# Kernel optimization log

Measured on AMD Instinct MI355X. Metric: run time of the kernel, lower is better.

Reference implementation:

```python
import jax, jax.numpy as jnp
import numpy as np

N = 256          # HiPPO order
DT = 1.0 / 4096  # discretization step ~ 1/L
L, BATCH = 4096, 64
GBT_ALPHA = 0.5  # bilinear transform (matches discretization=0.5)


def _legt_matrices(n):
    # Closed-form HiPPO-LegT transition matrices (Gu et al.), lambda_n=1.
    q = np.arange(n, dtype=np.float64)
    r = (2.0 * q + 1.0) ** 0.5
    j, i = np.meshgrid(q, q)  # i: row index n, j: col index k
    A = -(r[:, None] * np.where(i < j, (-1.0) ** (i - j), 1.0) * r[None, :])
    B = r[:, None]  # (N, 1)
    return A, B


def _discretize_gbt(A, B, dt, alpha):
    # Generalized bilinear transform, identical to scipy cont2discrete('gbt').
    n = A.shape[0]
    I = np.eye(n)
    M = np.linalg.inv(I - dt * alpha * A)
    dA = M @ (I + dt * (1.0 - alpha) * A)
    dB = (M @ (dt * B)).squeeze(-1)
    return dA.astype(np.float32), dB.astype(np.float32)


def setup_inputs() -> dict:
    key = jax.random.key(0)
    A, B = _legt_matrices(N)
    dA, dB = _discretize_gbt(A, B, DT, GBT_ALPHA)
    inputs = jax.random.normal(key, (L, BATCH), dtype=jnp.float32)
    return {"inputs": inputs, "dA": jnp.asarray(dA), "dB": jnp.asarray(dB)}


def reference(inputs, dA, dB):
    # inputs: (L, B); dA: (N, N); dB: (N,)
    # u_t = inputs_t[..., None] * dB  -> (L, B, N)
    u = inputs[..., None] * dB

    def step(c, u_t):
        # c_t = dA @ c_{t-1} + u_t  (row-vector form: c @ dA^T)
        c = c @ dA.T + u_t
        return c, c

    c0 = jnp.zeros(u.shape[1:], dtype=u.dtype)  # (B, N)
    _, cs = jax.lax.scan(step, c0, u)
    return cs  # (L, B, N)
```

## Files before the change

### kernel.cpp

```cpp
#include <hip/hip_runtime.h>
#include <hip/hip_bf16.h>
#include <stdint.h>


#define N 256
#define LSEQ 4096
#define BATCH 64
#define TCH 64
#define NCH 64

#define MG_STRIDE 36

using bf16x8 = __attribute__((ext_vector_type(8))) __bf16;
using f32x4  = __attribute__((ext_vector_type(4))) float;

__device__ __forceinline__ unsigned short f2bf(float f) {
  uint32_t x = __builtin_bit_cast(uint32_t, f);
  uint32_t r = x + 0x7fffu + ((x >> 16) & 1u);
  return (unsigned short)(r >> 16);
}
__device__ __forceinline__ float bf2f(unsigned short h) {
  uint32_t x = ((uint32_t)h) << 16;
  return __builtin_bit_cast(float, x);
}

__device__ __forceinline__ int swz(int r, int c) { return r * 32 + ((c ^ ((r >> 1) & 3)) << 3); }

#define OFF_Phi 16777216
#define OFF_Plo 25165824
#define OFF_Kf  33554432
#define OFF_Khi 33619968
#define OFF_Klo 33652736
#define OFF_shi 33685504
#define OFF_slo 35782656
#define OFF_G0  37879808
#define OFF_uT  42074112
#define OFF_Sqh 43122688
#define OFF_Sql 43778048


__device__ __forceinline__ void mm64_tile(const float* __restrict__ A, const float* __restrict__ B,
                                          float* __restrict__ Cw, unsigned short* __restrict__ Chi,
                                          unsigned short* __restrict__ Clo, int bx, int tid,
                                          char* smem) {
  float (*At)[68] = (float(*)[68])smem;
  float (*Bs)[68] = (float(*)[68])(smem + 4352);
  int gr0 = (bx >> 2) * 64, gc0 = (bx & 3) * 64;
  int ty = tid >> 4, tx = tid & 15;
  float acc[4][4];
  #pragma unroll
  for (int r = 0; r < 4; ++r)
    #pragma unroll
    for (int c = 0; c < 4; ++c) acc[r][c] = 0.f;
  int ra = tid >> 2, ka4 = (tid & 3) << 2;
  int kb = tid >> 4, cb4 = (tid & 15) << 2;
  const float* pa = &A[(size_t)(gr0 + ra) * 256 + ka4];
  const float* pb = &B[(size_t)kb * 256 + gc0 + cb4];
  float4 va = *(const float4*)pa;
  float4 vb = *(const float4*)pb;
  for (int k0 = 0; k0 < 256; k0 += 16) {
    At[ka4 + 0][ra] = va.x; At[ka4 + 1][ra] = va.y;
    At[ka4 + 2][ra] = va.z; At[ka4 + 3][ra] = va.w;
    *(float4*)&Bs[kb][cb4] = vb;
    __syncthreads();
    if (k0 + 16 < 256) {
      va = *(const float4*)(pa + k0 + 16);
      vb = *(const float4*)(pb + (size_t)(k0 + 16) * 256);
    }
    #pragma unroll
    for (int kk = 0; kk < 16; ++kk) {
      float4 a4 = *(const float4*)&At[kk][ty << 2];
      float4 b4 = *(const float4*)&Bs[kk][tx << 2];
      acc[0][0] += a4.x * b4.x; acc[0][1] += a4.x * b4.y; acc[0][2] += a4.x * b4.z; acc[0][3] += a4.x * b4.w;
      acc[1][0] += a4.y * b4.x; acc[1][1] += a4.y * b4.y; acc[1][2] += a4.y * b4.z; acc[1][3] += a4.y * b4.w;
      acc[2][0] += a4.z * b4.x; acc[2][1] += a4.z * b4.y; acc[2][2] += a4.z * b4.z; acc[2][3] += a4.z * b4.w;
      acc[3][0] += a4.w * b4.x; acc[3][1] += a4.w * b4.y; acc[3][2] += a4.w * b4.z; acc[3][3] += a4.w * b4.w;
    }
    __syncthreads();
  }
  #pragma unroll
  for (int r = 0; r < 4; ++r)
    #pragma unroll
    for (int c = 0; c < 4; ++c) {
      size_t idx = (size_t)(gr0 + ty * 4 + r) * 256 + gc0 + tx * 4 + c;
      float v = acc[r][c];
      Cw[idx] = v;
      unsigned short h = f2bf(v);
      Chi[idx] = h;
      Clo[idx] = f2bf(v - bf2f(h));
    }
}

__device__ __forceinline__ void finals_one(const float* __restrict__ Kf, const float* __restrict__ u,
                                           float* __restrict__ G0, int k, int b, int i) {
  float acc = 0.f;
  int ubase = (k * TCH + 63) * BATCH + b;
  #pragma unroll 8
  for (int p = 0; p < TCH; ++p)
    acc += Kf[p * N + i] * u[ubase - p * BATCH];
  G0[(size_t)(k * BATCH + b) * N + i] = acc;
}

template <int FINAL>
__device__ __forceinline__ void ks_tile(int bx, int tid, const float* __restrict__ Gin,
                                        float* __restrict__ Gout,
                                        const unsigned short* __restrict__ Mh,
                                        const unsigned short* __restrict__ Ml, int shift,
                                        unsigned short* __restrict__ shi,
                                        unsigned short* __restrict__ slo, char* smem) {
  unsigned short* Ah = (unsigned short*)smem;
  unsigned short* Al = (unsigned short*)(smem + 4096);
  unsigned short* Bh = (unsigned short*)(smem + 8192);
  unsigned short* Bl = (unsigned short*)(smem + 12288);
  int kb0 = (bx >> 2) * 64, i0 = (bx & 3) * 64;
  int lane = tid & 63, wid = tid >> 6;
  int wr = wid >> 1, wc = wid & 1;
  int rg = lane >> 4, cl = lane & 15;

  f32x4 acc[2][2];
  #pragma unroll
  for (int mf = 0; mf < 2; ++mf) {
    int m0 = kb0 + wr * 32 + mf * 16 + rg * 4;
    #pragma unroll
    for (int nf = 0; nf < 2; ++nf) {
      int i = i0 + wc * 32 + nf * 16 + cl;
      #pragma unroll
      for (int r = 0; r < 4; ++r)
        acc[mf][nf][r] = Gin[(size_t)(m0 + r) * 256 + i];
    }
  }

  int sr = tid >> 2, kc = tid & 3;
  int sw = swz(sr, kc);
  int srow = kb0 + sr - shift;
  bool haveA = (srow >= 0);
  const float* srcA = &Gin[(size_t)(haveA ? srow : 0) * 256 + kc * 8];
  const unsigned short* srcBh = &Mh[(size_t)(i0 + sr) * 256 + kc * 8];
  const unsigned short* srcBl = &Ml[(size_t)(i0 + sr) * 256 + kc * 8];

  float4 rA0, rA1;
  uint4 rBh = *(const uint4*)srcBh, rBl = *(const uint4*)srcBl;
  if (haveA) { rA0 = *(const float4*)srcA; rA1 = *(const float4*)(srcA + 4); }

  for (int kt = 0; kt < 8; ++kt) {
    if (haveA) {
      float vv[8] = {rA0.x, rA0.y, rA0.z, rA0.w, rA1.x, rA1.y, rA1.z, rA1.w};
      unsigned short hv[8], lv[8];
      #pragma unroll
      for (int e = 0; e < 8; ++e) {
        hv[e] = f2bf(vv[e]);
        lv[e] = f2bf(vv[e] - bf2f(hv[e]));
      }
      *(uint4*)&Ah[sw] = *(const uint4*)hv;
      *(uint4*)&Al[sw] = *(const uint4*)lv;
    } else {
      uint4 z = {0, 0, 0, 0};
      *(uint4*)&Ah[sw] = z;
      *(uint4*)&Al[sw] = z;
    }
    *(uint4*)&Bh[sw] = rBh;
    *(uint4*)&Bl[sw] = rBl;
    __syncthreads();

    if (kt < 7) {
      int off = (kt + 1) * 32;
      if (haveA) { rA0 = *(const float4*)(srcA + off); rA1 = *(const float4*)(srcA + off + 4); }
      rBh = *(const uint4*)(srcBh + off);
      rBl = *(const uint4*)(srcBl + off);
    }

    int fr = lane & 15, kseg = lane >> 4;
    bf16x8 ah[2], al[2], bh[2], bl[2];
    #pragma unroll
    for (int mf = 0; mf < 2; ++mf) {
      int row = wr * 32 + mf * 16 + fr;
      ah[mf] = *(const bf16x8*)&Ah[swz(row, kseg)];
      al[mf] = *(const bf16x8*)&Al[swz(row, kseg)];
    }
    #pragma unroll
    for (int nf = 0; nf < 2; ++nf) {
      int row = wc * 32 + nf * 16 + fr;
      bh[nf] = *(const bf16x8*)&Bh[swz(row, kseg)];
      bl[nf] = *(const bf16x8*)&Bl[swz(row, kseg)];
    }
    #pragma unroll
    for (int mf = 0; mf < 2; ++mf)
      #pragma unroll
      for (int nf = 0; nf < 2; ++nf) {
        acc[mf][nf] = __builtin_amdgcn_mfma_f32_16x16x32_bf16(ah[mf], bh[nf], acc[mf][nf], 0, 0, 0);
        acc[mf][nf] = __builtin_amdgcn_mfma_f32_16x16x32_bf16(ah[mf], bl[nf], acc[mf][nf], 0, 0, 0);
        acc[mf][nf] = __builtin_amdgcn_mfma_f32_16x16x32_bf16(al[mf], bh[nf], acc[mf][nf], 0, 0, 0);
      }
    __syncthreads();
  }

  #pragma unroll
  for (int mf = 0; mf < 2; ++mf) {
    int m0 = kb0 + wr * 32 + mf * 16 + rg * 4;
    #pragma unroll
    for (int nf = 0; nf < 2; ++nf) {
      int i = i0 + wc * 32 + nf * 16 + cl;
      #pragma unroll
      for (int r = 0; r < 4; ++r) {
        if (FINAL) {
          int tm = m0 + r + 64;
          if (tm < 4096) {
            float v = acc[mf][nf][r];
            unsigned short h = f2bf(v);
            shi[(size_t)tm * 256 + i] = h;
            slo[(size_t)tm * 256 + i] = f2bf(v - bf2f(h));
          }
        } else {
          Gout[(size_t)(m0 + r) * 256 + i] = acc[mf][nf][r];
        }
      }
    }
  }
  if (FINAL && kb0 == 0) {
    for (int e = tid; e < 4096; e += 256) {
      size_t o = (size_t)(e >> 6) * 256 + i0 + (e & 63);
      shi[o] = 0;
      slo[o] = 0;
    }
  }
}


__global__ __launch_bounds__(256) void prep0(const float* __restrict__ u, const float* __restrict__ dA,
                                             const float* __restrict__ dB,
                                             float* __restrict__ uT, float* __restrict__ Pw,
                                             unsigned short* __restrict__ Phi, unsigned short* __restrict__ Plo,
                                             float* __restrict__ Kf, unsigned short* __restrict__ Khi,
                                             unsigned short* __restrict__ Klo) {
  __shared__ float tile[64][65];
  int bid = blockIdx.x, tid = threadIdx.x;
  if (bid < 64) {
    int t0 = bid * 64;
    #pragma unroll
    for (int q = 0; q < 16; ++q) {
      int e = q * 256 + tid;
      int tt = e >> 6, b = e & 63;
      tile[b][tt] = u[(size_t)(t0 + tt) * 64 + b];
    }
    __syncthreads();
    #pragma unroll
    for (int q = 0; q < 16; ++q) {
      int e = q * 256 + tid;
      int b = e >> 6, tt = e & 63;
      uT[(size_t)b * 4096 + t0 + tt] = tile[b][tt];
    }
  } else if (bid < 128) {
    int base = (bid - 64) * 1024 + tid * 4;
    float4 v = *(const float4*)&dA[base];
    *(float4*)&Pw[base] = v;
    float vv[4] = {v.x, v.y, v.z, v.w};
    #pragma unroll
    for (int q = 0; q < 4; ++q) {
      unsigned short h = f2bf(vv[q]);
      Phi[base + q] = h;
      Plo[base + q] = f2bf(vv[q] - bf2f(h));
    }
  } else {
    float v = dB[tid];
    Kf[tid] = v;
    unsigned short h = f2bf(v);
    Khi[tid] = h;
    Klo[tid] = f2bf(v - bf2f(h));
  }
}

__global__ __launch_bounds__(256) void pow_K(float* __restrict__ Pw,
                                             unsigned short* __restrict__ Phi,
                                             unsigned short* __restrict__ Plo,
                                             float* __restrict__ Kf,
                                             unsigned short* __restrict__ Khi,
                                             unsigned short* __restrict__ Klo,
                                             int half) {
  __shared__ __align__(16) char smem[16640];
  int bx = blockIdx.x, tid = threadIdx.x;
  if (bx < 16 * half) {
    int q = (bx >> 4) + 1, t = bx & 15;
    mm64_tile(Pw + (size_t)(q - 1) * 65536, Pw + (size_t)(half - 1) * 65536,
              Pw + (size_t)(half + q - 1) * 65536, Phi + (size_t)(half + q - 1) * 65536,
              Plo + (size_t)(half + q - 1) * 65536, t, tid, smem);
  } else {
    int r = bx - 16 * half;
    int jp = r >> 2, quarter = r & 3;
    int p = half + jp;
    const float* M = Pw + (size_t)(half - 1) * 65536;
    const float* v = Kf + (size_t)jp * 256;
    int lane = tid & 63, w = tid >> 6;
    float d0 = v[lane], d1 = v[lane + 64], d2 = v[lane + 128], d3 = v[lane + 192];
    for (int ii = 0; ii < 16; ++ii) {
      int i = quarter * 64 + w * 16 + ii;
      const float* row = M + (size_t)i * 256;
      float acc = row[lane] * d0 + row[lane + 64] * d1 + row[lane + 128] * d2 + row[lane + 192] * d3;
      #pragma unroll
      for (int off = 32; off; off >>= 1) acc += __shfl_xor(acc, off, 64);
      if (lane == 0) {
        Kf[p * 256 + i] = acc;
        unsigned short h = f2bf(acc);
        Khi[p * 256 + i] = h;
        Klo[p * 256 + i] = f2bf(acc - bf2f(h));
      }
    }
  }
}

__global__ __launch_bounds__(256) void finals_sq(const float* __restrict__ Kf, const float* __restrict__ u,
                                                 float* __restrict__ G0,
                                                 const float* __restrict__ S0, float* __restrict__ S1,
                                                 unsigned short* __restrict__ Sqh0,
                                                 unsigned short* __restrict__ Sql0) {
  __shared__ __align__(16) char smem[16640];
  if (blockIdx.x < 64) {
    finals_one(Kf, u, G0, blockIdx.x, blockIdx.y, threadIdx.x);
  } else if (blockIdx.y < 16) {
    mm64_tile(S0, S0, S1, Sqh0, Sql0, blockIdx.y, threadIdx.x, smem);
  }
}

template <int FINAL>
__global__ __launch_bounds__(256) void ks_level(const float* __restrict__ Gin, float* __restrict__ Gout,
                                                const unsigned short* __restrict__ Mh,
                                                const unsigned short* __restrict__ Ml, int shift,
                                                unsigned short* __restrict__ shi,
                                                unsigned short* __restrict__ slo,
                                                const float* __restrict__ SqA, float* __restrict__ SqC,
                                                unsigned short* __restrict__ SqChi,
                                                unsigned short* __restrict__ SqClo) {
  __shared__ __align__(16) char smem[16640];
  int bx = blockIdx.x;
  if (bx < 256) {
    ks_tile<FINAL>(bx, threadIdx.x, Gin, Gout, Mh, Ml, shift, shi, slo, smem);
  } else {
    mm64_tile(SqA, SqA, SqC, SqChi, SqClo, bx - 256, threadIdx.x, smem);
  }
}

__global__ __launch_bounds__(256, 2) void main_gemm(const unsigned short* __restrict__ shi,
                                                    const unsigned short* __restrict__ slo,
                                                    const unsigned short* __restrict__ Phi,
                                                    const unsigned short* __restrict__ Plo,
                                                    const unsigned short* __restrict__ Khi,
                                                    const unsigned short* __restrict__ Klo,
                                                    const float* __restrict__ uT,
                                                    float* __restrict__ out) {
  __shared__ unsigned short Ah[128 * MG_STRIDE], Al[128 * MG_STRIDE];
  __shared__ unsigned short Bh[128 * MG_STRIDE], Bl[128 * MG_STRIDE];
  int dt = blockIdx.y;
  int x = blockIdx.x;
  int it = x >> 5, kbt = x & 31;
  int kb0 = kbt * 128, i0 = it * 128;
  int tid = threadIdx.x;
  int lane = tid & 63, wid = tid >> 6;
  int wr = wid >> 1, wc = wid & 1;

  f32x4 acc[4][4];
  #pragma unroll
  for (int mf = 0; mf < 4; ++mf)
    #pragma unroll
    for (int nf = 0; nf < 4; ++nf)
      #pragma unroll
      for (int r = 0; r < 4; ++r) acc[mf][nf][r] = 0.f;

  const unsigned short* PhiD = Phi + (size_t)dt * 65536;
  const unsigned short* PloD = Plo + (size_t)dt * 65536;
  int nkt = (dt >= 32) ? 10 : 9;

  int r = tid >> 1, h = tid & 1;
  int lo_ = r * MG_STRIDE + h * 16;
  const unsigned short* b1 = shi  + (size_t)(kb0 + r) * 256 + h * 16;
  const unsigned short* b2 = slo  + (size_t)(kb0 + r) * 256 + h * 16;
  const unsigned short* b3 = PhiD + (size_t)(i0 + r) * 256 + h * 16;
  const unsigned short* b4 = PloD + (size_t)(i0 + r) * 256 + h * 16;
  uint4 r1a = *(const uint4*)b1;
  uint4 r1b = *(const uint4*)(b1 + 8);
  uint4 r2a = *(const uint4*)b2;
  uint4 r2b = *(const uint4*)(b2 + 8);
  uint4 r3a = *(const uint4*)b3;
  uint4 r3b = *(const uint4*)(b3 + 8);
  uint4 r4a = *(const uint4*)b4;
  uint4 r4b = *(const uint4*)(b4 + 8);

  for (int kt = 0; kt < nkt; ++kt) {
    if (kt < 8) {
      *(uint4*)&Ah[lo_]     = r1a;
      *(uint4*)&Ah[lo_ + 8] = r1b;
      *(uint4*)&Al[lo_]     = r2a;
      *(uint4*)&Al[lo_ + 8] = r2b;
      *(uint4*)&Bh[lo_]     = r3a;
      *(uint4*)&Bh[lo_ + 8] = r3b;
      *(uint4*)&Bl[lo_]     = r4a;
      *(uint4*)&Bl[lo_ + 8] = r4b;
    } else {
      int p0 = (kt - 8) * 32;
      int kk = (kb0 + r) >> 6, b = (kb0 + r) & 63;
      const float* ub2 = uT + (size_t)b * 4096 + kk * 64 + dt;
      #pragma unroll
      for (int qq = 0; qq < 16; ++qq) {
        int pp = h * 16 + qq;
        int sh = p0 + pp;
        float v = (sh <= dt) ? ub2[-sh] : 0.f;
        unsigned short hv = f2bf(v);
        Ah[r * MG_STRIDE + pp] = hv;
        Al[r * MG_STRIDE + pp] = f2bf(v - bf2f(hv));
      }
      int n = tid & 127, ph = tid >> 7;
      #pragma unroll
      for (int qq = 0; qq < 16; ++qq) {
        int pp = ph * 16 + qq;
        Bh[n * MG_STRIDE + pp] = Khi[(p0 + pp) * 256 + i0 + n];
        Bl[n * MG_STRIDE + pp] = Klo[(p0 + pp) * 256 + i0 + n];
      }
    }
    __syncthreads();

    if (kt + 1 < 8) {
      int co = (kt + 1) * 32;
      r1a = *(const uint4*)(b1 + co);
      r1b = *(const uint4*)(b1 + co + 8);
      r2a = *(const uint4*)(b2 + co);
      r2b = *(const uint4*)(b2 + co + 8);
      r3a = *(const uint4*)(b3 + co);
      r3b = *(const uint4*)(b3 + co + 8);
      r4a = *(const uint4*)(b4 + co);
      r4b = *(const uint4*)(b4 + co + 8);
    }

    int kseg = lane >> 4, fr = lane & 15;
    bf16x8 ah[4], al[4], bh[4], bl[4];
    #pragma unroll
    for (int mf = 0; mf < 4; ++mf) {
      int row = (wr * 64 + mf * 16 + fr) * MG_STRIDE + kseg * 8;
      ah[mf] = *(const bf16x8*)&Ah[row];
      al[mf] = *(const bf16x8*)&Al[row];
    }
    #pragma unroll
    for (int nf = 0; nf < 4; ++nf) {
      int row = (wc * 64 + nf * 16 + fr) * MG_STRIDE + kseg * 8;
      bh[nf] = *(const bf16x8*)&Bh[row];
      bl[nf] = *(const bf16x8*)&Bl[row];
    }
    #pragma unroll
    for (int mf = 0; mf < 4; ++mf)
      #pragma unroll
      for (int nf = 0; nf < 4; ++nf) {
        acc[mf][nf] = __builtin_amdgcn_mfma_f32_16x16x32_bf16(ah[mf], bh[nf], acc[mf][nf], 0, 0, 0);
        acc[mf][nf] = __builtin_amdgcn_mfma_f32_16x16x32_bf16(ah[mf], bl[nf], acc[mf][nf], 0, 0, 0);
        acc[mf][nf] = __builtin_amdgcn_mfma_f32_16x16x32_bf16(al[mf], bh[nf], acc[mf][nf], 0, 0, 0);
      }
    __syncthreads();
  }

  int rg = lane >> 4, cl = lane & 15;
  #pragma unroll
  for (int mf = 0; mf < 4; ++mf) {
    int kbrow_base = kb0 + wr * 64 + mf * 16 + rg * 4;
    #pragma unroll
    for (int nf = 0; nf < 4; ++nf) {
      int i = i0 + wc * 64 + nf * 16 + cl;
      #pragma unroll
      for (int rr = 0; rr < 4; ++rr) {
        int kbrow = kbrow_base + rr;
        int k = kbrow >> 6, b = kbrow & 63;
        size_t t = (size_t)(k * 64 + dt);
        out[(t * 64 + b) * 256 + i] = acc[mf][nf][rr];
      }
    }
  }
}


extern "C" void kernel_launch(void* const* d_in, const int* in_sizes, int n_in,
                              void* d_out, int out_size, void* d_ws, size_t ws_size,
                              hipStream_t stream) {
  (void)in_sizes; (void)n_in; (void)out_size;
  const float* u  = (const float*)d_in[0];
  const float* dA = (const float*)d_in[1];
  const float* dB = (const float*)d_in[2];
  float* out = (float*)d_out;
  char* ws = (char*)d_ws;

  float*          Pw  = (float*)(ws);
  unsigned short* Phi = (unsigned short*)(ws + OFF_Phi);
  unsigned short* Plo = (unsigned short*)(ws + OFF_Plo);
  float*          Kf  = (float*)(ws + OFF_Kf);
  unsigned short* Khi = (unsigned short*)(ws + OFF_Khi);
  unsigned short* Klo = (unsigned short*)(ws + OFF_Klo);
  unsigned short* shi = (unsigned short*)(ws + OFF_shi);
  unsigned short* slo = (unsigned short*)(ws + OFF_slo);
  float*          G0  = (float*)(ws + OFF_G0);
  unsigned short* Sqh = (unsigned short*)(ws + OFF_Sqh);
  unsigned short* Sql = (unsigned short*)(ws + OFF_Sql);

  const size_t NEED_KS = 44433408;
  if (ws_size < NEED_KS) return;

  float* G1 = (float*)ws;

  float* S[6];
  S[0] = Pw + (size_t)63 * 65536;
  for (int d = 1; d <= 5; ++d) S[d] = Pw + (size_t)(55 + d) * 65536;

  prep0<<<129, 256, 0, stream>>>(u, dA, dB, (float*)(ws + OFF_uT), Pw, Phi, Plo, Kf, Khi, Klo);
  for (int half = 1; half <= 32; half <<= 1)
    pow_K<<<20 * half, 256, 0, stream>>>(Pw, Phi, Plo, Kf, Khi, Klo, half);

  finals_sq<<<dim3(65, 64), 256, 0, stream>>>(Kf, u, G0, S[0], S[1], Sqh, Sql);

  const unsigned short* Mh0 = Phi + (size_t)63 * 65536;
  const unsigned short* Ml0 = Plo + (size_t)63 * 65536;
  ks_level<0><<<272, 256, 0, stream>>>(G0, G1, Mh0, Ml0, 64, nullptr, nullptr,
                                       S[1], S[2], Sqh + 1 * 65536, Sql + 1 * 65536);
  ks_level<0><<<272, 256, 0, stream>>>(G1, G0, Sqh + 0 * 65536, Sql + 0 * 65536, 128, nullptr, nullptr,
                                       S[2], S[3], Sqh + 2 * 65536, Sql + 2 * 65536);
  ks_level<0><<<272, 256, 0, stream>>>(G0, G1, Sqh + 1 * 65536, Sql + 1 * 65536, 256, nullptr, nullptr,
                                       S[3], S[4], Sqh + 3 * 65536, Sql + 3 * 65536);
  ks_level<0><<<272, 256, 0, stream>>>(G1, G0, Sqh + 2 * 65536, Sql + 2 * 65536, 512, nullptr, nullptr,
                                       S[4], S[5], Sqh + 4 * 65536, Sql + 4 * 65536);
  ks_level<0><<<256, 256, 0, stream>>>(G0, G1, Sqh + 3 * 65536, Sql + 3 * 65536, 1024, nullptr, nullptr,
                                       nullptr, nullptr, nullptr, nullptr);
  ks_level<1><<<256, 256, 0, stream>>>(G1, nullptr, Sqh + 4 * 65536, Sql + 4 * 65536, 2048, shi, slo,
                                       nullptr, nullptr, nullptr, nullptr);

  main_gemm<<<dim3(64, 64), 256, 0, stream>>>(shi, slo, Phi, Plo, Khi, Klo,
                                              (const float*)(ws + OFF_uT), out);
}
```

Before: 334.0 us.

## Store scan state in MFMA fragment order and load A operand directly to registers

The final ks_level pass now writes the hi/lo bf16 split state in a pre-swizzled layout that matches the per-wave MFMA A-fragment order. main_gemm then loads its A operand straight from global memory into registers, prefetching one k-step ahead, instead of staging it through shared memory. This removes the A-side LDS writes and reads in the first eight k-steps. In exchange the per-wave global loads carry no cross-wave reuse, and two kernels now depend on the same custom layout.

Measured after the change: 378.2 us. +13.2%, slower.

```diff
diff --git a/kernel.cpp b/kernel.cpp
--- a/kernel.cpp
+++ b/kernel.cpp
@@ -25,6 +25,7 @@
 }
 
 __device__ __forceinline__ int swz(int r, int c) { return r * 32 + ((c ^ ((r >> 1) & 3)) << 3); }
+
 
 #define OFF_Phi 16777216
 #define OFF_Plo 25165824
@@ -207,8 +208,12 @@
           if (tm < 4096) {
             float v = acc[mf][nf][r];
             unsigned short h = f2bf(v);
-            shi[(size_t)tm * 256 + i] = h;
-            slo[(size_t)tm * 256 + i] = f2bf(v - bf2f(h));
+            int kbt = tm >> 7, wrf = (tm >> 6) & 1, mff = (tm >> 4) & 3, frf = tm & 15;
+            int jt = i >> 5, ks2 = (i >> 3) & 3, e = i & 7;
+            size_t idx = ((((size_t)(kbt * 8 + jt) * 2 + wrf) * 4 + mff) * 64
+                          + ks2 * 16 + frf) * 8 + e;
+            shi[idx] = h;
+            slo[idx] = f2bf(v - bf2f(h));
           }
         } else {
           Gout[(size_t)(m0 + r) * 256 + i] = acc[mf][nf][r];
@@ -217,10 +222,12 @@
     }
   }
   if (FINAL && kb0 == 0) {
+    int jt0 = (bx & 3) * 2;
     for (int e = tid; e < 4096; e += 256) {
-      size_t o = (size_t)(e >> 6) * 256 + i0 + (e & 63);
-      shi[o] = 0;
-      slo[o] = 0;
+      int jt = jt0 + (e >> 11);
+      size_t idx = (size_t)jt * 4096 + (e & 2047);
+      shi[idx] = 0;
+      slo[idx] = 0;
     }
   }
 }
@@ -338,8 +345,8 @@
   }
 }
 
-__global__ __launch_bounds__(256, 2) void main_gemm(const unsigned short* __restrict__ shi,
-                                                    const unsigned short* __restrict__ slo,
+__global__ __launch_bounds__(256, 2) void main_gemm(const unsigned short* __restrict__ sfh,
+                                                    const unsigned short* __restrict__ sfl,
                                                     const unsigned short* __restrict__ Phi,
                                                     const unsigned short* __restrict__ Plo,
                                                     const unsigned short* __restrict__ Khi,
@@ -370,25 +377,24 @@
 
   int r = tid >> 1, h = tid & 1;
   int lo_ = r * MG_STRIDE + h * 16;
-  const unsigned short* b1 = shi  + (size_t)(kb0 + r) * 256 + h * 16;
-  const unsigned short* b2 = slo  + (size_t)(kb0 + r) * 256 + h * 16;
   const unsigned short* b3 = PhiD + (size_t)(i0 + r) * 256 + h * 16;
   const unsigned short* b4 = PloD + (size_t)(i0 + r) * 256 + h * 16;
-  uint4 r1a = *(const uint4*)b1;
-  uint4 r1b = *(const uint4*)(b1 + 8);
-  uint4 r2a = *(const uint4*)b2;
-  uint4 r2b = *(const uint4*)(b2 + 8);
   uint4 r3a = *(const uint4*)b3;
   uint4 r3b = *(const uint4*)(b3 + 8);
   uint4 r4a = *(const uint4*)b4;
   uint4 r4b = *(const uint4*)(b4 + 8);
 
+  const unsigned short* afh = sfh + (size_t)(kbt * 8) * 4096 + wr * 2048 + lane * 8;
+  const unsigned short* afl = sfl + (size_t)(kbt * 8) * 4096 + wr * 2048 + lane * 8;
+  bf16x8 pah[4], pal[4];
+  #pragma unroll
+  for (int mf = 0; mf < 4; ++mf) {
+    pah[mf] = *(const bf16x8*)&afh[mf * 512];
+    pal[mf] = *(const bf16x8*)&afl[mf * 512];
+  }
+
   for (int kt = 0; kt < nkt; ++kt) {
     if (kt < 8) {
-      *(uint4*)&Ah[lo_]     = r1a;
-      *(uint4*)&Ah[lo_ + 8] = r1b;
-      *(uint4*)&Al[lo_]     = r2a;
-      *(uint4*)&Al[lo_ + 8] = r2b;
       *(uint4*)&Bh[lo_]     = r3a;
       *(uint4*)&Bh[lo_ + 8] = r3b;
       *(uint4*)&Bl[lo_]     = r4a;
@@ -418,10 +424,6 @@
 
     if (kt + 1 < 8) {
       int co = (kt + 1) * 32;
-      r1a = *(const uint4*)(b1 + co);
-      r1b = *(const uint4*)(b1 + co + 8);
-      r2a = *(const uint4*)(b2 + co);
-      r2b = *(const uint4*)(b2 + co + 8);
       r3a = *(const uint4*)(b3 + co);
       r3b = *(const uint4*)(b3 + co + 8);
       r4a = *(const uint4*)(b4 + co);
@@ -430,11 +432,25 @@
 
     int kseg = lane >> 4, fr = lane & 15;
     bf16x8 ah[4], al[4], bh[4], bl[4];
-    #pragma unroll
-    for (int mf = 0; mf < 4; ++mf) {
-      int row = (wr * 64 + mf * 16 + fr) * MG_STRIDE + kseg * 8;
-      ah[mf] = *(const bf16x8*)&Ah[row];
-      al[mf] = *(const bf16x8*)&Al[row];
+    if (kt < 8) {
+      #pragma unroll
+      for (int mf = 0; mf < 4; ++mf) { ah[mf] = pah[mf]; al[mf] = pal[mf]; }
+      if (kt + 1 < 8) {
+        const unsigned short* nh = afh + (size_t)(kt + 1) * 4096;
+        const unsigned short* nl = afl + (size_t)(kt + 1) * 4096;
+        #pragma unroll
+        for (int mf = 0; mf < 4; ++mf) {
+          pah[mf] = *(const bf16x8*)&nh[mf * 512];
+          pal[mf] = *(const bf16x8*)&nl[mf * 512];
+        }
+      }
+    } else {
+      #pragma unroll
+      for (int mf = 0; mf < 4; ++mf) {
+        int row = (wr * 64 + mf * 16 + fr) * MG_STRIDE + kseg * 8;
+        ah[mf] = *(const bf16x8*)&Ah[row];
+        al[mf] = *(const bf16x8*)&Al[row];
+      }
     }
     #pragma unroll
     for (int nf = 0; nf < 4; ++nf) {
```

## Double-buffer LDS tiles in main_gemm and prefetch two k-steps ahead

Applied to the files above, without the earlier changes.

Converts the main GEMM's shared-memory A/B tiles into two ping-pong buffers so the next k-tile is stored to LDS while the current one is consumed by MFMAs. This drops one of the two barriers per k-iteration, and the global loads are issued two steps ahead. The tail iterations that build the Toeplitz input correction remain single-buffered. LDS use doubles to about 73 KB per block, which may limit residency to fewer than the requested two blocks per CU.

New measurement: 346.2 us. 1.04x slower.

```diff
diff --git a/kernel.cpp b/kernel.cpp
--- a/kernel.cpp
+++ b/kernel.cpp
@@ -10,6 +10,7 @@
 #define NCH 64
 
 #define MG_STRIDE 36
+#define MG_SZ (128 * MG_STRIDE)
 
 using bf16x8 = __attribute__((ext_vector_type(8))) __bf16;
 using f32x4  = __attribute__((ext_vector_type(4))) float;
@@ -346,8 +347,8 @@
                                                     const unsigned short* __restrict__ Klo,
                                                     const float* __restrict__ uT,
                                                     float* __restrict__ out) {
-  __shared__ unsigned short Ah[128 * MG_STRIDE], Al[128 * MG_STRIDE];
-  __shared__ unsigned short Bh[128 * MG_STRIDE], Bl[128 * MG_STRIDE];
+  __shared__ unsigned short AhB[2 * MG_SZ], AlB[2 * MG_SZ];
+  __shared__ unsigned short BhB[2 * MG_SZ], BlB[2 * MG_SZ];
   int dt = blockIdx.y;
   int x = blockIdx.x;
   int it = x >> 5, kbt = x & 31;
@@ -355,6 +356,7 @@
   int tid = threadIdx.x;
   int lane = tid & 63, wid = tid >> 6;
   int wr = wid >> 1, wc = wid & 1;
+  int kseg = lane >> 4, fr = lane & 15;
 
   f32x4 acc[4][4];
   #pragma unroll
@@ -374,27 +376,64 @@
   const unsigned short* b2 = slo  + (size_t)(kb0 + r) * 256 + h * 16;
   const unsigned short* b3 = PhiD + (size_t)(i0 + r) * 256 + h * 16;
   const unsigned short* b4 = PloD + (size_t)(i0 + r) * 256 + h * 16;
-  uint4 r1a = *(const uint4*)b1;
-  uint4 r1b = *(const uint4*)(b1 + 8);
-  uint4 r2a = *(const uint4*)b2;
-  uint4 r2b = *(const uint4*)(b2 + 8);
-  uint4 r3a = *(const uint4*)b3;
-  uint4 r3b = *(const uint4*)(b3 + 8);
-  uint4 r4a = *(const uint4*)b4;
-  uint4 r4b = *(const uint4*)(b4 + 8);
-
-  for (int kt = 0; kt < nkt; ++kt) {
-    if (kt < 8) {
-      *(uint4*)&Ah[lo_]     = r1a;
-      *(uint4*)&Ah[lo_ + 8] = r1b;
-      *(uint4*)&Al[lo_]     = r2a;
-      *(uint4*)&Al[lo_ + 8] = r2b;
-      *(uint4*)&Bh[lo_]     = r3a;
-      *(uint4*)&Bh[lo_ + 8] = r3b;
-      *(uint4*)&Bl[lo_]     = r4a;
-      *(uint4*)&Bl[lo_ + 8] = r4b;
-    } else {
-      int p0 = (kt - 8) * 32;
+
+  uint4 r1a = *(const uint4*)b1, r1b = *(const uint4*)(b1 + 8);
+  uint4 r2a = *(const uint4*)b2, r2b = *(const uint4*)(b2 + 8);
+  uint4 r3a = *(const uint4*)b3, r3b = *(const uint4*)(b3 + 8);
+  uint4 r4a = *(const uint4*)b4, r4b = *(const uint4*)(b4 + 8);
+  *(uint4*)&AhB[lo_] = r1a;  *(uint4*)&AhB[lo_ + 8] = r1b;
+  *(uint4*)&AlB[lo_] = r2a;  *(uint4*)&AlB[lo_ + 8] = r2b;
+  *(uint4*)&BhB[lo_] = r3a;  *(uint4*)&BhB[lo_ + 8] = r3b;
+  *(uint4*)&BlB[lo_] = r4a;  *(uint4*)&BlB[lo_ + 8] = r4b;
+  r1a = *(const uint4*)(b1 + 32); r1b = *(const uint4*)(b1 + 40);
+  r2a = *(const uint4*)(b2 + 32); r2b = *(const uint4*)(b2 + 40);
+  r3a = *(const uint4*)(b3 + 32); r3b = *(const uint4*)(b3 + 40);
+  r4a = *(const uint4*)(b4 + 32); r4b = *(const uint4*)(b4 + 40);
+  __syncthreads();
+
+  for (int kt = 0; kt < 8; ++kt) {
+    int cc = (kt & 1) * MG_SZ;
+    int cn = MG_SZ - cc;
+    bf16x8 ah[4], al[4], bh[4], bl[4];
+    #pragma unroll
+    for (int mf = 0; mf < 4; ++mf) {
+      int row = cc + (wr * 64 + mf * 16 + fr) * MG_STRIDE + kseg * 8;
+      ah[mf] = *(const bf16x8*)&AhB[row];
+      al[mf] = *(const bf16x8*)&AlB[row];
+    }
+    #pragma unroll
+    for (int nf = 0; nf < 4; ++nf) {
+      int row = cc + (wc * 64 + nf * 16 + fr) * MG_STRIDE + kseg * 8;
+      bh[nf] = *(const bf16x8*)&BhB[row];
+      bl[nf] = *(const bf16x8*)&BlB[row];
+    }
+    if (kt < 7) {
+      *(uint4*)&AhB[cn + lo_] = r1a;  *(uint4*)&AhB[cn + lo_ + 8] = r1b;
+      *(uint4*)&AlB[cn + lo_] = r2a;  *(uint4*)&AlB[cn + lo_ + 8] = r2b;
+      *(uint4*)&BhB[cn + lo_] = r3a;  *(uint4*)&BhB[cn + lo_ + 8] = r3b;
+      *(uint4*)&BlB[cn + lo_] = r4a;  *(uint4*)&BlB[cn + lo_ + 8] = r4b;
+    }
+    if (kt < 6) {
+      int co = (kt + 2) * 32;
+      r1a = *(const uint4*)(b1 + co); r1b = *(const uint4*)(b1 + co + 8);
+      r2a = *(const uint4*)(b2 + co); r2b = *(const uint4*)(b2 + co + 8);
+      r3a = *(const uint4*)(b3 + co); r3b = *(const uint4*)(b3 + co + 8);
+      r4a = *(const uint4*)(b4 + co); r4b = *(const uint4*)(b4 + co + 8);
+    }
+    #pragma unroll
+    for (int mf = 0; mf < 4; ++mf)
+      #pragma unroll
+      for (int nf = 0; nf < 4; ++nf) {
+        acc[mf][nf] = __builtin_amdgcn_mfma_f32_16x16x32_bf16(ah[mf], bh[nf], acc[mf][nf], 0, 0, 0);
+        acc[mf][nf] = __builtin_amdgcn_mfma_f32_16x16x32_bf16(ah[mf], bl[nf], acc[mf][nf], 0, 0, 0);
+        acc[mf][nf] = __builtin_amdgcn_mfma_f32_16x16x32_bf16(al[mf], bh[nf], acc[mf][nf], 0, 0, 0);
+      }
+    __syncthreads();
+  }
+
+  for (int kt = 8; kt < nkt; ++kt) {
+    int p0 = (kt - 8) * 32;
+    {
       int kk = (kb0 + r) >> 6, b = (kb0 + r) & 63;
       const float* ub2 = uT + (size_t)b * 4096 + kk * 64 + dt;
       #pragma unroll
@@ -403,44 +442,30 @@
         int sh = p0 + pp;
         float v = (sh <= dt) ? ub2[-sh] : 0.f;
         unsigned short hv = f2bf(v);
-        Ah[r * MG_STRIDE + pp] = hv;
-        Al[r * MG_STRIDE + pp] = f2bf(v - bf2f(hv));
+        AhB[r * MG_STRIDE + pp] = hv;
+        AlB[r * MG_STRIDE + pp] = f2bf(v - bf2f(hv));
       }
       int n = tid & 127, ph = tid >> 7;
       #pragma unroll
       for (int qq = 0; qq < 16; ++qq) {
         int pp = ph * 16 + qq;
-        Bh[n * MG_STRIDE + pp] = Khi[(p0 + pp) * 256 + i0 + n];
-        Bl[n * MG_STRIDE + pp] = Klo[(p0 + pp) * 256 + i0 + n];
-      }
-    }
-    __syncthreads();
-
-    if (kt + 1 < 8) {
-      int co = (kt + 1) * 32;
-      r1a = *(const uint4*)(b1 + co);
-      r1b = *(const uint4*)(b1 + co + 8);
-      r2a = *(const uint4*)(b2 + co);
-      r2b = *(const uint4*)(b2 + co + 8);
-      r3a = *(const uint4*)(b3 + co);
-      r3b = *(const uint4*)(b3 + co + 8);
-      r4a = *(const uint4*)(b4 + co);
-      r4b = *(const uint4*)(b4 + co + 8);
-    }
-
-    int kseg = lane >> 4, fr = lane & 15;
+        BhB[n * MG_STRIDE + pp] = Khi[(p0 + pp) * 256 + i0 + n];
+        BlB[n * MG_STRIDE + pp] = Klo[(p0 + pp) * 256 + i0 + n];
+      }
+    }
+    __syncthreads();
     bf16x8 ah[4], al[4], bh[4], bl[4];
     #pragma unroll
     for (int mf = 0; mf < 4; ++mf) {
       int row = (wr * 64 + mf * 16 + fr) * MG_STRIDE + kseg * 8;
-      ah[mf] = *(const bf16x8*)&Ah[row];
-      al[mf] = *(const bf16x8*)&Al[row];
+      ah[mf] = *(const bf16x8*)&AhB[row];
+      al[mf] = *(const bf16x8*)&AlB[row];
     }
     #pragma unroll
     for (int nf = 0; nf < 4; ++nf) {
       int row = (wc * 64 + nf * 16 + fr) * MG_STRIDE + kseg * 8;
-      bh[nf] = *(const bf16x8*)&Bh[row];
-      bl[nf] = *(const bf16x8*)&Bl[row];
+      bh[nf] = *(const bf16x8*)&BhB[row];
+      bl[nf] = *(const bf16x8*)&BlB[row];
     }
     #pragma unroll
     for (int mf = 0; mf < 4; ++mf)
```
